# Optimization experiments

Hardware: AMD Instinct MI355X
Metric: run time of the kernel (lower is better)

## Reference

```python
import jax, jax.numpy as jnp
import numpy as np

N, F, H, E, P = 2048, 128, 32, 65536, 768

def _layer_norm(v, g, b, eps=1e-5):
    mu = v.mean(-1, keepdims=True)
    var = v.var(-1, keepdims=True)
    return (v - mu) / jnp.sqrt(var + eps) * g + b

def _gcn_conv(h, src, dst, W, b, n):
    # PyG GCNConv: add self-loops, sym-normalized aggregation, then bias
    h = h @ W
    loop = jnp.arange(n)
    s = jnp.concatenate([src, loop])
    d = jnp.concatenate([dst, loop])
    deg = jax.ops.segment_sum(jnp.ones_like(s, jnp.float32), d, num_segments=n)
    dinv = jnp.where(deg > 0, deg ** -0.5, 0.0)
    msg = h[s] * (dinv[s] * dinv[d])[:, None]
    return jax.ops.segment_sum(msg, d, num_segments=n) + b

def setup_inputs():
    key = jax.random.key(0)
    ks = jax.random.split(key, 16)
    def nrm(i, shape, scale=0.05):
        return jax.random.normal(ks[i], shape, jnp.float32) * scale
    return {
        "x": jax.random.normal(ks[0], (N, F), jnp.float32),
        "ei": jax.random.randint(ks[1], (2, E), 0, N),
        "pos": jax.random.randint(ks[2], (2, P), 0, N),
        "W1": nrm(3, (F, H)), "b1": jnp.zeros((H,), jnp.float32),
        "W2": nrm(4, (H, H)), "b2": jnp.zeros((H,), jnp.float32),
        "m1_w": nrm(5, (H, H)), "m1_b": jnp.zeros((H,), jnp.float32),
        "m1_g": jnp.ones((H,), jnp.float32), "m1_beta": jnp.zeros((H,), jnp.float32),
        "m2_w": nrm(6, (H, H)), "m2_b": jnp.zeros((H,), jnp.float32),
        "m2_g": jnp.ones((H,), jnp.float32), "m2_beta": jnp.zeros((H,), jnp.float32),
        "m3_w1": nrm(7, (2 * H, H)), "m3_b1": jnp.zeros((H,), jnp.float32),
        "m3_w2": nrm(8, (H, 1)), "m3_b2": jnp.zeros((1,), jnp.float32),
    }

def reference(x, ei, pos, W1, b1, W2, b2, m1_w, m1_b, m1_g, m1_beta,
              m2_w, m2_b, m2_g, m2_beta, m3_w1, m3_b1, m3_w2, m3_b2):
    src, dst = ei[0], ei[1]
    h = _gcn_conv(x, src, dst, W1, b1, N)
    h = _gcn_conv(h, src, dst, W2, b2, N)
    xx = h[pos[0]] * h[pos[1]]          # [P,H] pair products
    xe = h[src] * h[dst]                # [E,H] edge products
    # mlp1/mlp2: Linear -> LayerNorm -> Dropout(eval: identity) -> ReLU
    x1 = jax.nn.relu(_layer_norm(xe @ m1_w + m1_b, m1_g, m1_beta))  # right factor
    x2 = jax.nn.relu(_layer_norm(xe @ m2_w + m2_b, m2_g, m2_beta))  # left factor (mlp2)
    # Scatter edge features into per-channel adjacency matrices [H,N,N]
    A1 = jnp.zeros((H, N, N), jnp.float32).at[:, src, dst].set(x2.T)
    A2 = jnp.zeros((H, N, N), jnp.float32).at[:, src, dst].set(x1.T)
    # C = bmm(A1, A2); combine() only reads C at pos pairs (zeros elsewhere),
    # so gather the needed rows/cols and contract -- identical math, no NxN output.
    rows = A1[:, pos[0], :]             # [H,P,N]
    cols = A2[:, :, pos[1]]             # [H,N,P]
    pos_val = jnp.einsum('hpn,hnp->ph', rows, cols)   # [P,H]
    z = jnp.concatenate([pos_val, xx], axis=1)        # [P,2H]
    z = jax.nn.relu(z @ m3_w1 + m3_b1)
    return (z @ m3_w2 + m3_b2).squeeze(-1)            # [P]
```

## Files before the change

kernel.cpp:

```cpp
#include <hip/hip_runtime.h>

#define N_NODES 2048
#define F_IN    128
#define HD      32
#define E_EDGES 65536
#define P_PAIRS 768

__global__ __launch_bounds__(256) void k_deg_mm1(const int* __restrict__ dst,
                                                 int* __restrict__ deg,
                                                 const float* __restrict__ x,
                                                 const float* __restrict__ W1,
                                                 float* __restrict__ hW) {
    __shared__ float sW[F_IN * HD];
    int tid = threadIdx.x;
    int bid = blockIdx.x;
    if (bid < 256) {
        int e = bid * 256 + tid;
        atomicAdd(&deg[dst[e]], 1);
        return;
    }
    const float4* W4 = (const float4*)W1;
    float4* s4 = (float4*)sW;
    for (int i = tid; i < F_IN * HD / 4; i += 256) s4[i] = W4[i];
    __syncthreads();
    int n = (bid - 256) * 8 + (tid >> 5), j = tid & 31;
    const float4* row = (const float4*)(x + n * F_IN);
    float acc = 0.f;
#pragma unroll
    for (int k4 = 0; k4 < F_IN / 4; ++k4) {
        float4 r = row[k4];
        acc = fmaf(r.x, sW[(k4 * 4 + 0) * HD + j], acc);
        acc = fmaf(r.y, sW[(k4 * 4 + 1) * HD + j], acc);
        acc = fmaf(r.z, sW[(k4 * 4 + 2) * HD + j], acc);
        acc = fmaf(r.w, sW[(k4 * 4 + 3) * HD + j], acc);
    }
    hW[n * HD + j] = acc;
}

__global__ __launch_bounds__(256) void k_scan(const int* __restrict__ deg, float* __restrict__ dinv,
                       int* __restrict__ offs, int* __restrict__ cursor) {
    __shared__ int ps[256];
    int tid = threadIdx.x;
    int base = tid * 8;
    int local[8]; int s = 0;
#pragma unroll
    for (int q = 0; q < 8; ++q) {
        int dg = deg[base + q];
        local[q] = s; s += dg;
        dinv[base + q] = 1.0f / sqrtf((float)(dg + 1));
    }
    ps[tid] = s; __syncthreads();
    for (int d = 1; d < 256; d <<= 1) {
        int t = (tid >= d) ? ps[tid - d] : 0;
        __syncthreads();
        ps[tid] += t;
        __syncthreads();
    }
    int excl = ps[tid] - s;
#pragma unroll
    for (int q = 0; q < 8; ++q) {
        offs[base + q]   = excl + local[q];
        cursor[base + q] = excl + local[q];
    }
    if (tid == 0) offs[N_NODES] = E_EDGES;
}

__global__ __launch_bounds__(256) void k_csr(const int* __restrict__ src, const int* __restrict__ dst,
                      const float* __restrict__ dinv,
                      int* __restrict__ cursor,
                      int* __restrict__ csr_s, float* __restrict__ csr_w,
                      int* __restrict__ eid, int* __restrict__ eidT) {
    int e = blockIdx.x * 256 + threadIdx.x;
    int s = src[e], d = dst[e];
    int p = atomicAdd(&cursor[d], 1);
    csr_s[p] = s;
    csr_w[p] = dinv[s] * dinv[d];
    atomicMax(&eid [(size_t)s * N_NODES + d], e);
    atomicMax(&eidT[(size_t)d * N_NODES + s], e);
}

__device__ __forceinline__ float csr_gather(const float* __restrict__ H,
                                            const int* __restrict__ csr_s,
                                            const float* __restrict__ csr_w,
                                            int beg, int end, int j) {
    float acc = 0.f;
    int p = beg;
    for (; p + 4 <= end; p += 4) {
        int   s0 = csr_s[p],   s1 = csr_s[p+1], s2 = csr_s[p+2], s3 = csr_s[p+3];
        float w0 = csr_w[p],   w1 = csr_w[p+1], w2 = csr_w[p+2], w3 = csr_w[p+3];
        float h0 = H[s0 * HD + j], h1 = H[s1 * HD + j];
        float h2 = H[s2 * HD + j], h3 = H[s3 * HD + j];
        acc = fmaf(h0, w0, acc);
        acc = fmaf(h1, w1, acc);
        acc = fmaf(h2, w2, acc);
        acc = fmaf(h3, w3, acc);
    }
    for (; p < end; ++p)
        acc = fmaf(H[csr_s[p] * HD + j], csr_w[p], acc);
    return acc;
}

__global__ __launch_bounds__(256) void k_gcn1mm2(const float* __restrict__ hW, const int* __restrict__ offs,
                          const int* __restrict__ csr_s, const float* __restrict__ csr_w,
                          const float* __restrict__ dinv, const float* __restrict__ b1,
                          const float* __restrict__ W2, float* __restrict__ hW2) {
    __shared__ float sW2[HD * HD];
    __shared__ float sH[8][HD];
    int tid = threadIdx.x;
    for (int i = tid; i < HD * HD; i += 256) sW2[i] = W2[i];
    __syncthreads();
    int nl = tid >> 5, j = tid & 31;
    int n = blockIdx.x * 8 + nl;
    float acc = csr_gather(hW, csr_s, csr_w, offs[n], offs[n + 1], j);
    float di = dinv[n];
    acc = fmaf(hW[n * HD + j], di * di, acc);
    sH[nl][j] = acc + b1[j];
    __syncthreads();
    float y = 0.f;
#pragma unroll
    for (int k = 0; k < HD; ++k)
        y = fmaf(sH[nl][k], sW2[k * HD + j], y);
    hW2[n * HD + j] = y;
}

__global__ __launch_bounds__(256) void k_gcn2(const float* __restrict__ hW2, const int* __restrict__ offs,
                       const int* __restrict__ csr_s, const float* __restrict__ csr_w,
                       const float* __restrict__ dinv, const float* __restrict__ b2,
                       float* __restrict__ h2) {
    int tid = threadIdx.x;
    int nl = tid >> 5, j = tid & 31;
    int n = blockIdx.x * 8 + nl;
    float acc = csr_gather(hW2, csr_s, csr_w, offs[n], offs[n + 1], j);
    float di = dinv[n];
    acc = fmaf(hW2[n * HD + j], di * di, acc);
    h2[n * HD + j] = acc + b2[j];
}

__global__ __launch_bounds__(256) void k_pos(const int* __restrict__ pos,
                      const int* __restrict__ eid, const int* __restrict__ eidT,
                      const int* __restrict__ src, const int* __restrict__ dst,
                      const float* __restrict__ h2,
                      const float* __restrict__ m1w, const float* __restrict__ m1b,
                      const float* __restrict__ m1g, const float* __restrict__ m1be,
                      const float* __restrict__ m2w, const float* __restrict__ m2b,
                      const float* __restrict__ m2g, const float* __restrict__ m2be,
                      const float* __restrict__ w1, const float* __restrict__ b1,
                      const float* __restrict__ w2, const float* __restrict__ b2,
                      float* __restrict__ out) {
    __shared__ float s_w1[HD * HD], s_w2[HD * HD];
    __shared__ int2  q[N_NODES];
    __shared__ int   qn;
    __shared__ float acc[HD];
    __shared__ float sz[2 * HD];
    int p = blockIdx.x;
    int i = pos[p], jn = pos[P_PAIRS + p];
    int tid = threadIdx.x;
    for (int t = tid; t < HD * HD; t += 256) { s_w1[t] = m1w[t]; s_w2[t] = m2w[t]; }
    if (tid == 0) qn = 0;
    if (tid < HD) acc[tid] = 0.f;
    __syncthreads();

    const int4* rowA = (const int4*)(eid  + (size_t)i  * N_NODES);
    const int4* rowB = (const int4*)(eidT + (size_t)jn * N_NODES);
    for (int t = tid; t < N_NODES / 4; t += 256) {
        int4 ea = rowA[t];
        int4 eb = rowB[t];
        int e1[4] = { ea.x, ea.y, ea.z, ea.w };
        int e2[4] = { eb.x, eb.y, eb.z, eb.w };
#pragma unroll
        for (int u = 0; u < 4; ++u) {
            if ((e1[u] | e2[u]) >= 0) {
                int slot = atomicAdd(&qn, 1);
                q[slot] = make_int2(e1[u], e2[u]);
            }
        }
    }
    __syncthreads();

    int nmatch = qn;
    int wave = tid >> 6;
    int j = tid & 31;
    float bb1 = m1b[j], bb2 = m2b[j];
    float g1v = m1g[j], g2v = m2g[j];
    float be1 = m1be[j], be2 = m2be[j];
    for (int m = wave; m < nmatch; m += 4) {
        int2 me = q[m];
        int e1 = me.x, e2 = me.y;
        int s1 = src[e1], d1 = dst[e1];
        int s2 = src[e2], d2 = dst[e2];
        float xeA = h2[s1 * HD + j] * h2[d1 * HD + j];
        float xeB = h2[s2 * HD + j] * h2[d2 * HD + j];
        float yA = bb2, yB = bb1;
#pragma unroll
        for (int k = 0; k < HD; ++k) {
            float ka = __shfl(xeA, k, 32);
            float kb = __shfl(xeB, k, 32);
            yA = fmaf(ka, s_w2[k * HD + j], yA);
            yB = fmaf(kb, s_w1[k * HD + j], yB);
        }
        float muA = yA, muB = yB;
#pragma unroll
        for (int mm = 16; mm > 0; mm >>= 1) { muA += __shfl_xor(muA, mm, 32); muB += __shfl_xor(muB, mm, 32); }
        muA *= (1.f / 32.f); muB *= (1.f / 32.f);
        float dA = yA - muA, dB = yB - muB;
        float vA = dA * dA, vB = dB * dB;
#pragma unroll
        for (int mm = 16; mm > 0; mm >>= 1) { vA += __shfl_xor(vA, mm, 32); vB += __shfl_xor(vB, mm, 32); }
        vA *= (1.f / 32.f); vB *= (1.f / 32.f);
        float x2v = fmaxf(dA / sqrtf(vA + 1e-5f) * g2v + be2, 0.f);
        float x1v = fmaxf(dB / sqrtf(vB + 1e-5f) * g1v + be1, 0.f);
        if ((tid & 63) < 32) atomicAdd(&acc[j], x2v * x1v);
    }
    __syncthreads();

    if (tid < HD) {
        sz[tid] = acc[tid];
        sz[HD + tid] = h2[i * HD + tid] * h2[jn * HD + tid];
    }
    __syncthreads();
    if (tid < HD) {
        float t = b1[tid];
#pragma unroll
        for (int k = 0; k < 2 * HD; ++k) t = fmaf(sz[k], w1[k * HD + tid], t);
        t = fmaxf(t, 0.f);
        float r = t * w2[tid];
#pragma unroll
        for (int mm = 16; mm > 0; mm >>= 1) r += __shfl_xor(r, mm, 32);
        if (tid == 0) out[p] = r + b2[0];
    }
}

extern "C" void kernel_launch(void* const* d_in, const int* in_sizes, int n_in,
                              void* d_out, int out_size, void* d_ws, size_t ws_size,
                              hipStream_t stream) {
    const float* x     = (const float*)d_in[0];
    const int*   ei    = (const int*)d_in[1];
    const int*   pos   = (const int*)d_in[2];
    const float* W1    = (const float*)d_in[3];
    const float* b1    = (const float*)d_in[4];
    const float* W2    = (const float*)d_in[5];
    const float* b2    = (const float*)d_in[6];
    const float* m1w   = (const float*)d_in[7];
    const float* m1b   = (const float*)d_in[8];
    const float* m1g   = (const float*)d_in[9];
    const float* m1be  = (const float*)d_in[10];
    const float* m2w   = (const float*)d_in[11];
    const float* m2b   = (const float*)d_in[12];
    const float* m2g   = (const float*)d_in[13];
    const float* m2be  = (const float*)d_in[14];
    const float* m3w1  = (const float*)d_in[15];
    const float* m3b1  = (const float*)d_in[16];
    const float* m3w2  = (const float*)d_in[17];
    const float* m3b2  = (const float*)d_in[18];

    const int* src = ei;
    const int* dst = ei + E_EDGES;

    char* w = (char*)d_ws;
    size_t off = 0;
    auto alloc = [&](size_t bytes) { void* p = w + off; off += (bytes + 255) & ~size_t(255); return p; };
    int*   deg    = (int*)  alloc(N_NODES * 4);
    float* dinv   = (float*)alloc(N_NODES * 4);
    int*   offs   = (int*)  alloc((N_NODES + 1) * 4);
    int*   cursor = (int*)  alloc(N_NODES * 4);
    int*   csr_s  = (int*)  alloc((size_t)E_EDGES * 4);
    float* csr_w  = (float*)alloc((size_t)E_EDGES * 4);
    float* hW     = (float*)alloc((size_t)N_NODES * HD * 4);
    float* hW2    = (float*)alloc((size_t)N_NODES * HD * 4);
    float* h2     = (float*)alloc((size_t)N_NODES * HD * 4);
    int*   eid    = (int*)  alloc((size_t)N_NODES * N_NODES * 4);
    int*   eidT   = (int*)  alloc((size_t)N_NODES * N_NODES * 4);

    hipMemsetAsync(deg, 0, N_NODES * 4, stream);

    k_deg_mm1<<<512, 256, 0, stream>>>(dst, deg, x, W1, hW);
    k_scan<<<1, 256, 0, stream>>>(deg, dinv, offs, cursor);
    k_csr<<<E_EDGES / 256, 256, 0, stream>>>(src, dst, dinv, cursor, csr_s, csr_w, eid, eidT);

    k_gcn1mm2<<<N_NODES / 8, 256, 0, stream>>>(hW, offs, csr_s, csr_w, dinv, b1, W2, hW2);
    k_gcn2<<<N_NODES / 8, 256, 0, stream>>>(hW2, offs, csr_s, csr_w, dinv, b2, h2);

    k_pos<<<P_PAIRS, 256, 0, stream>>>(pos, eid, eidT, src, dst, h2,
                                       m1w, m1b, m1g, m1be, m2w, m2b, m2g, m2be,
                                       m3w1, m3b1, m3w2, m3b2, (float*)d_out);
}
```

Measured before the change: 142.3 us.

## Fuse degree histogram and scan into one block; filter eid atomics by pos bitmaps

The degree count, prefix scan and pair-node bitmaps now run in a single extra block of the first matmul kernel, using a shared-memory histogram. This removes the memset, the separate scan launch and the global degree atomics. The CSR kernel now performs the eid/eidT atomicMax scatter only for edges whose source or destination appears in the pos rows or columns, which cuts most random atomic traffic into the large N×N tables. In exchange, one block serially processes all 65536 edges for the histogram, which may become the critical path of that kernel.

```diff
diff --git a/kernel.cpp b/kernel.cpp
--- a/kernel.cpp
+++ b/kernel.cpp
@@ -6,77 +6,96 @@
 #define E_EDGES 65536
 #define P_PAIRS 768
 
-__global__ __launch_bounds__(256) void k_deg_mm1(const int* __restrict__ dst,
-                                                 int* __restrict__ deg,
-                                                 const float* __restrict__ x,
-                                                 const float* __restrict__ W1,
-                                                 float* __restrict__ hW) {
-    __shared__ float sW[F_IN * HD];
+union SmemK1 {
+    float sW[F_IN * HD];
+    struct { int hist[N_NODES]; int ps[256];
+             unsigned bm0[64]; unsigned bm1[64]; } prep;
+};
+
+__global__ __launch_bounds__(256) void k_mm1_prep(const float* __restrict__ x,
+                                                  const float* __restrict__ W1,
+                                                  float* __restrict__ hW,
+                                                  const int* __restrict__ dst,
+                                                  const int* __restrict__ pos,
+                                                  float* __restrict__ dinv,
+                                                  int* __restrict__ offs,
+                                                  int* __restrict__ cursor,
+                                                  unsigned* __restrict__ g_bm0,
+                                                  unsigned* __restrict__ g_bm1) {
+    __shared__ SmemK1 sm;
     int tid = threadIdx.x;
     int bid = blockIdx.x;
-    if (bid < 256) {
-        int e = bid * 256 + tid;
-        atomicAdd(&deg[dst[e]], 1);
+    if (bid == 256) {
+        for (int i = tid; i < N_NODES; i += 256) sm.prep.hist[i] = 0;
+        if (tid < 64) { sm.prep.bm0[tid] = 0u; sm.prep.bm1[tid] = 0u; }
+        __syncthreads();
+        for (int e = tid; e < E_EDGES; e += 256)
+            atomicAdd(&sm.prep.hist[dst[e]], 1);
+        for (int t = tid; t < P_PAIRS; t += 256) {
+            int i0 = pos[t];
+            int j0 = pos[P_PAIRS + t];
+            atomicOr(&sm.prep.bm0[i0 >> 5], 1u << (i0 & 31));
+            atomicOr(&sm.prep.bm1[j0 >> 5], 1u << (j0 & 31));
+        }
+        __syncthreads();
+        int base = tid * 8;
+        int local[8]; int s = 0;
+#pragma unroll
+        for (int q = 0; q < 8; ++q) {
+            int dg = sm.prep.hist[base + q];
+            local[q] = s; s += dg;
+            dinv[base + q] = 1.0f / sqrtf((float)(dg + 1));
+        }
+        sm.prep.ps[tid] = s; __syncthreads();
+        for (int d = 1; d < 256; d <<= 1) {
+            int t = (tid >= d) ? sm.prep.ps[tid - d] : 0;
+            __syncthreads();
+            sm.prep.ps[tid] += t;
+            __syncthreads();
+        }
+        int excl = sm.prep.ps[tid] - s;
+#pragma unroll
+        for (int q = 0; q < 8; ++q) {
+            offs[base + q]   = excl + local[q];
+            cursor[base + q] = excl + local[q];
+        }
+        if (tid == 0) offs[N_NODES] = E_EDGES;
+        if (tid < 64) { g_bm0[tid] = sm.prep.bm0[tid]; g_bm1[tid] = sm.prep.bm1[tid]; }
         return;
     }
     const float4* W4 = (const float4*)W1;
-    float4* s4 = (float4*)sW;
+    float4* s4 = (float4*)sm.sW;
     for (int i = tid; i < F_IN * HD / 4; i += 256) s4[i] = W4[i];
     __syncthreads();
-    int n = (bid - 256) * 8 + (tid >> 5), j = tid & 31;
+    int n = bid * 8 + (tid >> 5), j = tid & 31;
     const float4* row = (const float4*)(x + n * F_IN);
     float acc = 0.f;
 #pragma unroll
     for (int k4 = 0; k4 < F_IN / 4; ++k4) {
         float4 r = row[k4];
-        acc = fmaf(r.x, sW[(k4 * 4 + 0) * HD + j], acc);
-        acc = fmaf(r.y, sW[(k4 * 4 + 1) * HD + j], acc);
-        acc = fmaf(r.z, sW[(k4 * 4 + 2) * HD + j], acc);
-        acc = fmaf(r.w, sW[(k4 * 4 + 3) * HD + j], acc);
+        acc = fmaf(r.x, sm.sW[(k4 * 4 + 0) * HD + j], acc);
+        acc = fmaf(r.y, sm.sW[(k4 * 4 + 1) * HD + j], acc);
+        acc = fmaf(r.z, sm.sW[(k4 * 4 + 2) * HD + j], acc);
+        acc = fmaf(r.w, sm.sW[(k4 * 4 + 3) * HD + j], acc);
     }
     hW[n * HD + j] = acc;
-}
-
-__global__ __launch_bounds__(256) void k_scan(const int* __restrict__ deg, float* __restrict__ dinv,
-                       int* __restrict__ offs, int* __restrict__ cursor) {
-    __shared__ int ps[256];
-    int tid = threadIdx.x;
-    int base = tid * 8;
-    int local[8]; int s = 0;
-#pragma unroll
-    for (int q = 0; q < 8; ++q) {
-        int dg = deg[base + q];
-        local[q] = s; s += dg;
-        dinv[base + q] = 1.0f / sqrtf((float)(dg + 1));
-    }
-    ps[tid] = s; __syncthreads();
-    for (int d = 1; d < 256; d <<= 1) {
-        int t = (tid >= d) ? ps[tid - d] : 0;
-        __syncthreads();
-        ps[tid] += t;
-        __syncthreads();
-    }
-    int excl = ps[tid] - s;
-#pragma unroll
-    for (int q = 0; q < 8; ++q) {
-        offs[base + q]   = excl + local[q];
-        cursor[base + q] = excl + local[q];
-    }
-    if (tid == 0) offs[N_NODES] = E_EDGES;
 }
 
 __global__ __launch_bounds__(256) void k_csr(const int* __restrict__ src, const int* __restrict__ dst,
                       const float* __restrict__ dinv,
                       int* __restrict__ cursor,
                       int* __restrict__ csr_s, float* __restrict__ csr_w,
-                      int* __restrict__ eid, int* __restrict__ eidT) {
+                      int* __restrict__ eid, int* __restrict__ eidT,
+                      const unsigned* __restrict__ bm0, const unsigned* __restrict__ bm1) {
     int e = blockIdx.x * 256 + threadIdx.x;
     int s = src[e], d = dst[e];
     int p = atomicAdd(&cursor[d], 1);
     csr_s[p] = s;
     csr_w[p] = dinv[s] * dinv[d];
-    atomicMax(&eid [(size_t)s * N_NODES + d], e);
-    atomicMax(&eidT[(size_t)d * N_NODES + s], e);
+    if ((bm0[s >> 5] >> (s & 31)) & 1u)
+        atomicMax(&eid [(size_t)s * N_NODES + d], e);
+    if ((bm1[d >> 5] >> (d & 31)) & 1u)
+        atomicMax(&eidT[(size_t)d * N_NODES + s], e);
 }
 
 __device__ __forceinline__ float csr_gather(const float* __restrict__ H,
@@ -259,27 +278,24 @@
     char* w = (char*)d_ws;
     size_t off = 0;
     auto alloc = [&](size_t bytes) { void* p = w + off; off += (bytes + 255) & ~size_t(255); return p; };
-    int*   deg    = (int*)  alloc(N_NODES * 4);
-    float* dinv   = (float*)alloc(N_NODES * 4);
-    int*   offs   = (int*)  alloc((N_NODES + 1) * 4);
-    int*   cursor = (int*)  alloc(N_NODES * 4);
-    int*   csr_s  = (int*)  alloc((size_t)E_EDGES * 4);
-    float* csr_w  = (float*)alloc((size_t)E_EDGES * 4);
-    float* hW     = (float*)alloc((size_t)N_NODES * HD * 4);
-    float* hW2    = (float*)alloc((size_t)N_NODES * HD * 4);
-    float* h2     = (float*)alloc((size_t)N_NODES * HD * 4);
-    int*   eid    = (int*)  alloc((size_t)N_NODES * N_NODES * 4);
-    int*   eidT   = (int*)  alloc((size_t)N_NODES * N_NODES * 4);
-
-    hipMemsetAsync(deg, 0, N_NODES * 4, stream);
-
-    k_deg_mm1<<<512, 256, 0, stream>>>(dst, deg, x, W1, hW);
-    k_scan<<<1, 256, 0, stream>>>(deg, dinv, offs, cursor);
-    k_csr<<<E_EDGES / 256, 256, 0, stream>>>(src, dst, dinv, cursor, csr_s, csr_w, eid, eidT);
-
+    float*    dinv   = (float*)   alloc(N_NODES * 4);
+    int*      offs   = (int*)     alloc((N_NODES + 1) * 4);
+    int*      cursor = (int*)     alloc(N_NODES * 4);
+    unsigned* bm0    = (unsigned*)alloc(64 * 4);
+    unsigned* bm1    = (unsigned*)alloc(64 * 4);
+    int*      csr_s  = (int*)     alloc((size_t)E_EDGES * 4);
+    float*    csr_w  = (float*)   alloc((size_t)E_EDGES * 4);
+    float*    hW     = (float*)   alloc((size_t)N_NODES * HD * 4);
+    float*    hW2    = (float*)   alloc((size_t)N_NODES * HD * 4);
+    float*    h2     = (float*)   alloc((size_t)N_NODES * HD * 4);
+    int*      eid    = (int*)     alloc((size_t)N_NODES * N_NODES * 4);
+    int*      eidT   = (int*)     alloc((size_t)N_NODES * N_NODES * 4);
+
+    k_mm1_prep<<<257, 256, 0, stream>>>(x, W1, hW, dst, pos, dinv, offs, cursor, bm0, bm1);
+    k_csr<<<E_EDGES / 256, 256, 0, stream>>>(src, dst, dinv, cursor, csr_s, csr_w,
+                                             eid, eidT, bm0, bm1);
     k_gcn1mm2<<<N_NODES / 8, 256, 0, stream>>>(hW, offs, csr_s, csr_w, dinv, b1, W2, hW2);
     k_gcn2<<<N_NODES / 8, 256, 0, stream>>>(hW2, offs, csr_s, csr_w, dinv, b2, h2);
-
     k_pos<<<P_PAIRS, 256, 0, stream>>>(pos, eid, eidT, src, dst, h2,
                                        m1w, m1b, m1g, m1be, m2w, m2b, m2g, m2be,
                                        m3w1, m3b1, m3w2, m3b2, (float*)d_out);
```

Result: slower. 187.7 us (+32.0%).
